# Optimization experiments

Measured on AMD Instinct MI355X. Metric: run time of the kernel, lower is better.

The kernel has to match this reference:

```python
import jax, jax.numpy as jnp
import numpy as np

EMBED_DIM = 1024
NUM_HEADS = 16
HEAD_DIM = EMBED_DIM // NUM_HEADS
SCALING = HEAD_DIM ** -0.5


def setup_inputs() -> dict:
    key = jax.random.key(0)
    ks = jax.random.split(key, 9)
    T, B, E = 2048, 4, EMBED_DIM
    s = 0.02
    return {
        "query": jax.random.normal(ks[0], (T, B, E), dtype=jnp.float32),
        "Wq": jax.random.normal(ks[1], (E, E), dtype=jnp.float32) * s,
        "bq": jnp.zeros((E,), dtype=jnp.float32),
        "Wk": jax.random.normal(ks[2], (E, E), dtype=jnp.float32) * s,
        "bk": jnp.zeros((E,), dtype=jnp.float32),
        "Wv": jax.random.normal(ks[3], (E, E), dtype=jnp.float32) * s,
        "bv": jnp.zeros((E,), dtype=jnp.float32),
        "Wo": jax.random.normal(ks[4], (E, E), dtype=jnp.float32) * s,
        "bo": jnp.zeros((E,), dtype=jnp.float32),
    }


def reference(query, Wq, bq, Wk, bk, Wv, bv, Wo, bo):
    # query: [T, B, E]; torch Linear: x @ W.T + b
    T, B, E = query.shape
    H, D = NUM_HEADS, HEAD_DIM
    q = (query @ Wq.T + bq) * SCALING
    k = query @ Wk.T + bk
    v = query @ Wv.T + bv
    # [T, B, E] -> [B*H, T, D]
    def split_heads(x):
        return x.reshape(T, B * H, D).transpose(1, 0, 2)
    q, k, v = split_heads(q), split_heads(k), split_heads(v)
    attn_weights = jnp.einsum("btd,bsd->bts", q, k)  # [B*H, T, T]
    attn_probs = jax.nn.softmax(attn_weights, axis=-1)
    attn = jnp.einsum("bts,bsd->btd", attn_probs, v)  # [B*H, T, D]
    attn = attn.transpose(1, 0, 2).reshape(T, B, E)
    return attn @ Wo.T + bo
```

## Files before the change

kernel.cpp:

```cpp
#include <hip/hip_runtime.h>
#include <stdint.h>

#define TSEQ   2048
#define BATCH  4
#define NHEAD  16
#define HDIM   64
#define EMB    1024
#define MROWS  (TSEQ * BATCH)
#define QKV_N  (3 * EMB)
#define SCALE_Q 0.125f
#define LOG2E  1.4426950408889634f

typedef __bf16  bf16x8  __attribute__((ext_vector_type(8)));
typedef __bf16  bf16x2  __attribute__((ext_vector_type(2)));
typedef short   s16x8   __attribute__((ext_vector_type(8)));
typedef float   f32x4   __attribute__((ext_vector_type(4)));
typedef float   f32x16  __attribute__((ext_vector_type(16)));

__device__ __forceinline__ uint16_t b16c(float f) {
    __bf16 h = (__bf16)f;
    return __builtin_bit_cast(uint16_t, h);
}
__device__ __forceinline__ uint32_t pk2(float a, float b) {
    bf16x2 h; h[0] = (__bf16)a; h[1] = (__bf16)b;
    return __builtin_bit_cast(uint32_t, h);
}
__device__ __forceinline__ float exp2hw(float x) {
    float r; asm("v_exp_f32 %0, %1" : "=v"(r) : "v"(x)); return r;
}
__device__ __forceinline__ bf16x8 ldfrag(const uint16_t* p) {
    return __builtin_bit_cast(bf16x8, *(const s16x8*)p);
}
__device__ __forceinline__ f32x4 MFMA(bf16x8 a, bf16x8 b, f32x4 c) {
    return __builtin_amdgcn_mfma_f32_16x16x32_bf16(a, b, c, 0, 0, 0);
}
__device__ __forceinline__ f32x16 MFMA32(bf16x8 a, bf16x8 b, f32x16 c) {
    return __builtin_amdgcn_mfma_f32_32x32x16_bf16(a, b, c, 0, 0, 0);
}

#define GLOAD_LDS16(g, l) \
    __builtin_amdgcn_global_load_lds((const __attribute__((address_space(1))) void*)(g), \
                                     (__attribute__((address_space(3))) void*)(l), 16, 0, 0)

__global__ void cvt_f2b4(const float* __restrict__ src, uint16_t* __restrict__ dst, int n4) {
    int i = blockIdx.x * blockDim.x + threadIdx.x;
    if (i >= n4) return;
    float4 v = ((const float4*)src)[i];
    ushort4 o;
    o.x = b16c(v.x); o.y = b16c(v.y); o.z = b16c(v.z); o.w = b16c(v.w);
    ((ushort4*)dst)[i] = o;
}

__global__ void cvt_wqkv(const float* __restrict__ Wq, const float* __restrict__ Wk,
                         const float* __restrict__ Wv, const float* __restrict__ bq,
                         const float* __restrict__ bk, const float* __restrict__ bv,
                         uint16_t* __restrict__ Wqkv, float* __restrict__ bqkv, int n4) {
    int i = blockIdx.x * blockDim.x + threadIdx.x;
    if (i < QKV_N) {
        float bval;
        if (i < EMB)            bval = bq[i] * SCALE_Q;
        else if (i < 2 * EMB)   bval = bk[i - EMB];
        else                    bval = bv[i - 2 * EMB];
        bqkv[i] = bval;
    }
    if (i >= n4) return;
    int e = i * 4;
    int n = e >> 10;
    int k = e & 1023;
    const float* src; float sc;
    if (n < EMB)            { src = Wq + ((size_t)n << 10) + k;             sc = SCALE_Q; }
    else if (n < 2 * EMB)   { src = Wk + ((size_t)(n - EMB) << 10) + k;     sc = 1.f; }
    else                    { src = Wv + ((size_t)(n - 2 * EMB) << 10) + k; sc = 1.f; }
    float4 v = *(const float4*)src;
    ushort4 o;
    o.x = b16c(v.x * sc); o.y = b16c(v.y * sc); o.z = b16c(v.z * sc); o.w = b16c(v.w * sc);
    ((ushort4*)Wqkv)[i] = o;
}

template <typename CT>
__global__ __launch_bounds__(256) void gemm_bt(
        const uint16_t* __restrict__ A, const uint16_t* __restrict__ Bt,
        const float* __restrict__ bias, CT* __restrict__ C,
        int M, int N, int K, int tiles_n) {
    __shared__ uint16_t As[128 * 32];
    __shared__ uint16_t Bs[128 * 32];

    const int nwg = gridDim.x;
    const int bid0 = blockIdx.x;
    const int bid = (bid0 & 7) * (nwg >> 3) + (bid0 >> 3);
    const int tm = bid / tiles_n, tn = bid % tiles_n;
    const int tid = threadIdx.x;
    const int l = tid & 63, w = tid >> 6;
    const int wm = w >> 1, wn = w & 1;
    const int fr = l & 15, fq = l >> 4;

    f32x4 acc[4][4] = {};

    const int row_a = tid >> 2;
    const int kblk  = (tid & 3) << 3;
    const uint16_t* gA0 = A  + (size_t)(tm * 128 + row_a) * K + kblk;
    const uint16_t* gB0 = Bt + (size_t)(tn * 128 + row_a) * K + kblk;
    const uint16_t* gA1 = gA0 + (size_t)64 * K;
    const uint16_t* gB1 = gB0 + (size_t)64 * K;
    uint16_t* lA0 = As + w * 512;
    uint16_t* lA1 = As + 2048 + w * 512;
    uint16_t* lB0 = Bs + w * 512;
    uint16_t* lB1 = Bs + 2048 + w * 512;

    for (int k0 = 0; k0 < K; k0 += 32) {
        GLOAD_LDS16(gA0 + k0, lA0);
        GLOAD_LDS16(gA1 + k0, lA1);
        GLOAD_LDS16(gB0 + k0, lB0);
        GLOAD_LDS16(gB1 + k0, lB1);
        __syncthreads();

        bf16x8 a[4], b[4];
#pragma unroll
        for (int i = 0; i < 4; i++)
            a[i] = ldfrag(&As[(wm * 64 + i * 16 + fr) * 32 + fq * 8]);
#pragma unroll
        for (int i = 0; i < 4; i++)
            b[i] = ldfrag(&Bs[(wn * 64 + i * 16 + fr) * 32 + fq * 8]);
#pragma unroll
        for (int i = 0; i < 4; i++)
#pragma unroll
            for (int j = 0; j < 4; j++)
                acc[i][j] = MFMA(a[i], b[j], acc[i][j]);
        __syncthreads();
    }

#pragma unroll
    for (int j = 0; j < 4; j++) {
        const int col = tn * 128 + wn * 64 + j * 16 + fr;
        const float bv = bias[col];
#pragma unroll
        for (int i = 0; i < 4; i++) {
#pragma unroll
            for (int r = 0; r < 4; r++) {
                const int row = tm * 128 + wm * 64 + i * 16 + fq * 4 + r;
                const float v = acc[i][j][r] + bv;
                if constexpr (sizeof(CT) == 2) C[(size_t)row * N + col] = (CT)b16c(v);
                else                           C[(size_t)row * N + col] = (CT)v;
            }
        }
    }
}

__device__ __forceinline__ int swze(int row, int colE) {
    return (row << 6) + (colE ^ ((((row & 7) ^ ((row >> 3) & 7)) & 7) << 3));
}

__device__ __forceinline__ void softmax_half(
        f32x16& s0, f32x16& s1, float& mrun, float& lrun,
        f32x16& oa, f32x16& ob, bf16x8* pf) {
    float t0 = s0[0], t1 = s0[1], t2 = s0[2], t3 = s0[3];
#pragma unroll
    for (int i = 4; i < 16; i += 4) {
        t0 = fmaxf(t0, s0[i]);     t1 = fmaxf(t1, s0[i + 1]);
        t2 = fmaxf(t2, s0[i + 2]); t3 = fmaxf(t3, s0[i + 3]);
    }
#pragma unroll
    for (int i = 0; i < 16; i += 4) {
        t0 = fmaxf(t0, s1[i]);     t1 = fmaxf(t1, s1[i + 1]);
        t2 = fmaxf(t2, s1[i + 2]); t3 = fmaxf(t3, s1[i + 3]);
    }
    float mx = fmaxf(fmaxf(t0, t1), fmaxf(t2, t3));
    {
        auto rm = __builtin_amdgcn_permlane32_swap(__float_as_int(mx), __float_as_int(mx), false, false);
        mx = fmaxf(__int_as_float(rm[0]), __int_as_float(rm[1]));
    }
    if (!__all(mx <= mrun + 8.f)) {
        float mnew = fmaxf(mrun, mx);
        float scl = exp2hw((mrun - mnew) * LOG2E);
        mrun = mnew;
        lrun *= scl;
#pragma unroll
        for (int i = 0; i < 16; i++) { oa[i] *= scl; ob[i] *= scl; }
    }
    const float mm = mrun * LOG2E;
#pragma unroll
    for (int i = 0; i < 16; i++) s0[i] = exp2hw(__builtin_fmaf(s0[i], LOG2E, -mm));
#pragma unroll
    for (int i = 0; i < 16; i++) s1[i] = exp2hw(__builtin_fmaf(s1[i], LOG2E, -mm));
    float p0 = 0.f, p1 = 0.f, p2 = 0.f, p3 = 0.f;
#pragma unroll
    for (int i = 0; i < 16; i += 4) {
        p0 += s0[i]; p1 += s0[i + 1]; p2 += s0[i + 2]; p3 += s0[i + 3];
        p0 += s1[i]; p1 += s1[i + 1]; p2 += s1[i + 2]; p3 += s1[i + 3];
    }
    float rs = (p0 + p1) + (p2 + p3);
    {
        auto rr2 = __builtin_amdgcn_permlane32_swap(__float_as_int(rs), __float_as_int(rs), false, false);
        rs = __int_as_float(rr2[0]) + __int_as_float(rr2[1]);
    }
    lrun += rs;

    uint32_t pk[16];
#pragma unroll
    for (int rr = 0; rr < 8; rr++) {
        pk[rr]     = pk2(s0[2 * rr], s0[2 * rr + 1]);
        pk[8 + rr] = pk2(s1[2 * rr], s1[2 * rr + 1]);
    }
#pragma unroll
    for (int kt = 0; kt < 4; kt++) {
        const int b0 = (kt >> 1) * 8 + (kt & 1) * 4;
        auto r02 = __builtin_amdgcn_permlane32_swap((int)pk[b0 + 0], (int)pk[b0 + 2], false, false);
        auto r13 = __builtin_amdgcn_permlane32_swap((int)pk[b0 + 1], (int)pk[b0 + 3], false, false);
        union { uint32_t u[4]; bf16x8 v; } cv;
        cv.u[0] = (uint32_t)r02[0]; cv.u[1] = (uint32_t)r13[0];
        cv.u[2] = (uint32_t)r02[1]; cv.u[3] = (uint32_t)r13[1];
        pf[kt] = cv.v;
    }
}

__global__ __launch_bounds__(256, 2) void flash_attn3(
        const uint16_t* __restrict__ qkv, uint16_t* __restrict__ attnb) {
    __shared__ __align__(16) uint16_t smem[16384];
    uint16_t* k0p = smem;
    uint16_t* k1p = smem + 4096;
    uint16_t* v0p = smem + 8192;
    uint16_t* v1p = smem + 12288;

    int bid = (int)blockIdx.x;
    bid = (bid & 7) * 64 + (bid >> 3);
    const int head = bid >> 3;
    const int qt   = bid & 7;
    const int b    = head >> 4, h = head & 15;
    const int tid  = threadIdx.x;
    const int l  = tid & 63, w = tid >> 6;
    const int q5 = l & 31;
    const int hi = l >> 5;
    const size_t tstep = (size_t)64 * 4 * 3072;

    const int qrowA = qt * 256 + w * 64 + q5;
    const uint16_t* qbA = qkv + ((size_t)(qrowA * 4 + b)) * 3072 + h * 64 + hi * 8;
    const uint16_t* qbB = qbA + (size_t)32 * 4 * 3072;
    bf16x8 qA[4], qB[4];
#pragma unroll
    for (int s = 0; s < 4; s++) { qA[s] = ldfrag(qbA + 16 * s); qB[s] = ldfrag(qbB + 16 * s); }

    const int r0 = w * 16 + (l >> 3);
    const int r1 = r0 + 8;
    const int cu0 = (((l & 7) ^ ((r0 & 7) ^ ((r0 >> 3) & 7))) & 7) << 3;
    const int cu1 = (((l & 7) ^ ((r1 & 7) ^ ((r1 >> 3) & 7))) & 7) << 3;
    const uint16_t* gk0 = qkv + ((size_t)(r0 * 4 + b)) * 3072 + 1024 + h * 64 + cu0;
    const uint16_t* gk1 = qkv + ((size_t)(r1 * 4 + b)) * 3072 + 1024 + h * 64 + cu1;
    const int kdst0 = w * 1024;
    const int kdst1 = w * 1024 + 512;

    const int skv  = (tid >> 3) * 2;
    const int scol = (tid & 7) * 8;
    const uint16_t* gv = qkv + ((size_t)(skv * 4 + b)) * 3072 + 2048 + h * 64 + scol;
    int voff[8];
#pragma unroll
    for (int j2 = 0; j2 < 8; j2++)
        voff[j2] = (scol + j2) * 64 + (skv ^ ((((j2 ^ (scol >> 3)) & 7)) << 3));

    GLOAD_LDS16(gk0, k0p + kdst0);
    GLOAD_LDS16(gk1, k0p + kdst1);
    {
        uint4 a0 = *(const uint4*)gv;
        uint4 a1 = *(const uint4*)(gv + 12288);
        const uint16_t* e0 = (const uint16_t*)&a0;
        const uint16_t* e1 = (const uint16_t*)&a1;
#pragma unroll
        for (int j2 = 0; j2 < 8; j2++)
            *(uint32_t*)&v0p[voff[j2]] = (uint32_t)e0[j2] | ((uint32_t)e1[j2] << 16);
    }
    gk0 += tstep; gk1 += tstep; gv += tstep;
    __syncthreads();

    f32x16 o0 = {}, o1 = {}, o2 = {}, o3 = {};
    float mrunA = -1e30f, lrunA = 0.f, mrunB = -1e30f, lrunB = 0.f;

    for (int t = 0; t < 32; t++) {
        const uint16_t* kb = (t & 1) ? k1p : k0p;
        const uint16_t* vb = (t & 1) ? v1p : v0p;
        uint16_t* kn = (t & 1) ? k0p : k1p;
        uint16_t* vn = (t & 1) ? v0p : v1p;

        uint4 a0, a1;
        if (t < 31) {
            GLOAD_LDS16(gk0, kn + kdst0);
            GLOAD_LDS16(gk1, kn + kdst1);
            a0 = *(const uint4*)gv;
            a1 = *(const uint4*)(gv + 12288);
            gk0 += tstep; gk1 += tstep; gv += tstep;
        }

        f32x16 sA0 = {}, sA1 = {}, sB0 = {}, sB1 = {};
#pragma unroll
        for (int s = 0; s < 4; s++) {
            bf16x8 kf0 = ldfrag(&kb[swze(q5,      16 * s + 8 * hi)]);
            bf16x8 kf1 = ldfrag(&kb[swze(32 + q5, 16 * s + 8 * hi)]);
            sA0 = MFMA32(kf0, qA[s], sA0);
            sA1 = MFMA32(kf1, qA[s], sA1);
            sB0 = MFMA32(kf0, qB[s], sB0);
            sB1 = MFMA32(kf1, qB[s], sB1);
        }

        bf16x8 pfA[4], pfB[4];
        softmax_half(sA0, sA1, mrunA, lrunA, o0, o1, pfA);
        softmax_half(sB0, sB1, mrunB, lrunB, o2, o3, pfB);

#pragma unroll
        for (int kt = 0; kt < 4; kt++) {
            bf16x8 vf0 = ldfrag(&vb[swze(q5,      16 * kt + 8 * hi)]);
            bf16x8 vf1 = ldfrag(&vb[swze(32 + q5, 16 * kt + 8 * hi)]);
            o0 = MFMA32(vf0, pfA[kt], o0);
            o1 = MFMA32(vf1, pfA[kt], o1);
            o2 = MFMA32(vf0, pfB[kt], o2);
            o3 = MFMA32(vf1, pfB[kt], o3);
        }

        if (t < 31) {
            const uint16_t* e0 = (const uint16_t*)&a0;
            const uint16_t* e1 = (const uint16_t*)&a1;
#pragma unroll
            for (int j2 = 0; j2 < 8; j2++)
                *(uint32_t*)&vn[voff[j2]] = (uint32_t)e0[j2] | ((uint32_t)e1[j2] << 16);
        }
        __syncthreads();
    }

    uint16_t* OstA = smem + w * 4096;
    uint16_t* OstB = OstA + 2048;
#pragma unroll
    for (int half = 0; half < 2; half++) {
        uint16_t* Ost = half ? OstB : OstA;
        const float inv = 1.f / (half ? lrunB : lrunA);
#pragma unroll
        for (int dt = 0; dt < 2; dt++) {
            const f32x16& ov = half ? (dt ? o3 : o2) : (dt ? o1 : o0);
#pragma unroll
            for (int a = 0; a < 4; a++) {
#pragma unroll
                for (int cp = 0; cp < 2; cp++) {
                    const int r = a * 4 + cp * 2;
                    uint32_t dw = pk2(ov[r] * inv, ov[r + 1] * inv);
                    const int d0 = dt * 32 + a * 8 + hi * 4 + cp * 2;
                    *(uint32_t*)&Ost[swze(q5, d0)] = dw;
                }
            }
        }
    }
    const int rq = l >> 1;
#pragma unroll
    for (int half = 0; half < 2; half++) {
        uint16_t* Ost = half ? OstB : OstA;
        const int qrow2 = qt * 256 + w * 64 + half * 32 + rq;
        uint16_t* ob = attnb + ((size_t)(qrow2 * 4 + b)) * 1024 + h * 64;
#pragma unroll
        for (int i = 0; i < 4; i++) {
            const int c4 = (l & 1) * 4 + i;
            uint4 vv = *(const uint4*)&Ost[swze(rq, c4 * 8)];
            *(uint4*)(ob + c4 * 8) = vv;
        }
    }
}

extern "C" void kernel_launch(void* const* d_in, const int* in_sizes, int n_in,
                              void* d_out, int out_size, void* d_ws, size_t ws_size,
                              hipStream_t stream) {
    const float* X  = (const float*)d_in[0];
    const float* Wq = (const float*)d_in[1];
    const float* bq = (const float*)d_in[2];
    const float* Wk = (const float*)d_in[3];
    const float* bk = (const float*)d_in[4];
    const float* Wv = (const float*)d_in[5];
    const float* bv = (const float*)d_in[6];
    const float* Wo = (const float*)d_in[7];
    const float* bo = (const float*)d_in[8];
    float* out = (float*)d_out;

    uint8_t* ws = (uint8_t*)d_ws;
    uint16_t* Xbf   = (uint16_t*)(ws);
    uint16_t* Wqkv  = (uint16_t*)(ws + 16777216);
    uint16_t* Wobf  = (uint16_t*)(ws + 23068672);
    float*    bqkv  = (float*)   (ws + 25165824);
    uint16_t* qkv   = (uint16_t*)(ws + 25178112);
    uint16_t* attnb = (uint16_t*)(ws + 75509760);

    cvt_f2b4<<<(MROWS * EMB / 4 + 255) / 256, 256, 0, stream>>>(X, Xbf, MROWS * EMB / 4);
    cvt_f2b4<<<(EMB * EMB / 4 + 255) / 256, 256, 0, stream>>>(Wo, Wobf, EMB * EMB / 4);
    cvt_wqkv<<<(QKV_N * EMB / 4 + 255) / 256, 256, 0, stream>>>(
        Wq, Wk, Wv, bq, bk, bv, Wqkv, bqkv, QKV_N * EMB / 4);

    gemm_bt<uint16_t><<<(MROWS / 128) * (QKV_N / 128), 256, 0, stream>>>(
        Xbf, Wqkv, bqkv, qkv, MROWS, QKV_N, EMB, QKV_N / 128);

    flash_attn3<<<512, 256, 0, stream>>>(qkv, attnb);

    gemm_bt<float><<<(MROWS / 128) * (EMB / 128), 256, 0, stream>>>(
        attnb, Wobf, bo, out, MROWS, EMB, EMB, EMB / 128);
}
```

Baseline: 218.6 us.

## Add 256x256 four-stage pipelined QKV GEMM and interleave softmax with PV MFMAs

Replaces the generic 128x128 GEMM for the QKV projection with a dedicated 512-thread kernel using 256x256 tiles, 32x32x16 MFMAs, a four-deep global_load_lds ring buffer with explicit vmcnt waits, and priority boosts around the MFMA blocks. In the attention kernel, the PV MFMAs for the first query half are issued between the two softmax passes so matrix work overlaps the exp and max work, and the QK loop gets setprio. The softmax row max is rewritten as a chain of three-input maxes so it can map to v_max3. The larger tile raises LDS use (128KB) and register pressure, which may limit occupancy.

Result: no change. 219.2 us (+0.3%).

```diff
diff --git a/kernel.cpp b/kernel.cpp
--- a/kernel.cpp
+++ b/kernel.cpp
@@ -27,6 +27,9 @@
 }
 __device__ __forceinline__ float exp2hw(float x) {
     float r; asm("v_exp_f32 %0, %1" : "=v"(r) : "v"(x)); return r;
+}
+__device__ __forceinline__ float max3f(float a, float b, float c) {
+    return fmaxf(fmaxf(a, b), c);
 }
 __device__ __forceinline__ bf16x8 ldfrag(const uint16_t* p) {
     return __builtin_bit_cast(bf16x8, *(const s16x8*)p);
@@ -146,6 +149,110 @@
     }
 }
 
+#define SWZK(r) ((((r) & 3) ^ (((r) >> 2) & 3)))
+
+__global__ __launch_bounds__(512, 2) void gemm_qkv(
+        const uint16_t* __restrict__ A, const uint16_t* __restrict__ Bt,
+        const float* __restrict__ bias, uint16_t* __restrict__ C) {
+    __shared__ __align__(16) uint16_t lds[4 * 16384];
+
+    const int bid0 = blockIdx.x;
+    const int bid = (bid0 & 7) * 48 + (bid0 >> 3);
+    const int tm = bid / 12, tn = bid % 12;
+    const int tid = threadIdx.x;
+    const int w = tid >> 6, l = tid & 63;
+    const int wm = w >> 2, wn = w & 3;
+    const int l5 = l & 31, hi = l >> 5;
+
+    const uint16_t* gA[2]; const uint16_t* gB[2];
+    int ldsA[2], ldsB[2];
+#pragma unroll
+    for (int i = 0; i < 2; i++) {
+        int c = i * 512 + tid;
+        int row = c >> 2, fqp = c & 3;
+        gA[i] = A  + (size_t)(tm * 256 + row) * 1024 + ((fqp ^ SWZK(row)) * 8);
+        gB[i] = Bt + (size_t)(tn * 256 + row) * 1024 + ((fqp ^ SWZK(row)) * 8);
+        ldsA[i] = (i * 512 + w * 64) * 8;
+        ldsB[i] = 8192 + (i * 512 + w * 64) * 8;
+    }
+
+    int aoff[4][2], boff[2][2];
+#pragma unroll
+    for (int mf = 0; mf < 4; mf++) {
+        int row = wm * 128 + mf * 32 + l5;
+#pragma unroll
+        for (int ks = 0; ks < 2; ks++)
+            aoff[mf][ks] = row * 32 + (((ks * 2 + hi) ^ SWZK(row)) * 8);
+    }
+#pragma unroll
+    for (int nf = 0; nf < 2; nf++) {
+        int row = wn * 64 + nf * 32 + l5;
+#pragma unroll
+        for (int ks = 0; ks < 2; ks++)
+            boff[nf][ks] = 8192 + row * 32 + (((ks * 2 + hi) ^ SWZK(row)) * 8);
+    }
+
+    f32x16 acc[4][2] = {};
+
+#define STAGE_T(t, s)                                            \
+    {                                                            \
+        uint16_t* base_ = lds + (s) * 16384;                     \
+        GLOAD_LDS16(gA[0] + (t) * 32, base_ + ldsA[0]);          \
+        GLOAD_LDS16(gB[0] + (t) * 32, base_ + ldsB[0]);          \
+        GLOAD_LDS16(gA[1] + (t) * 32, base_ + ldsA[1]);          \
+        GLOAD_LDS16(gB[1] + (t) * 32, base_ + ldsB[1]);          \
+    }
+
+    STAGE_T(0, 0); STAGE_T(1, 1); STAGE_T(2, 2);
+    asm volatile("s_waitcnt vmcnt(8)" ::: "memory");
+    __builtin_amdgcn_s_barrier();
+    __builtin_amdgcn_sched_barrier(0);
+
+    for (int j = 0; j < 32; j++) {
+        const int s = j & 3;
+        if (j + 3 < 32) STAGE_T(j + 3, (j + 3) & 3);
+        const uint16_t* sl = lds + s * 16384;
+
+#pragma unroll
+        for (int ks = 0; ks < 2; ks++) {
+            bf16x8 af[4], bfg[2];
+#pragma unroll
+            for (int mf = 0; mf < 4; mf++) af[mf] = ldfrag(sl + aoff[mf][ks]);
+#pragma unroll
+            for (int nf = 0; nf < 2; nf++) bfg[nf] = ldfrag(sl + boff[nf][ks]);
+            __builtin_amdgcn_s_setprio(1);
+#pragma unroll
+            for (int mf = 0; mf < 4; mf++)
+#pragma unroll
+                for (int nf = 0; nf < 2; nf++)
+                    acc[mf][nf] = MFMA32(af[mf], bfg[nf], acc[mf][nf]);
+            __builtin_amdgcn_s_setprio(0);
+        }
+
+        __builtin_amdgcn_sched_barrier(0);
+        if (j < 29)       asm volatile("s_waitcnt vmcnt(8)" ::: "memory");
+        else if (j == 29) asm volatile("s_waitcnt vmcnt(4)" ::: "memory");
+        else              asm volatile("s_waitcnt vmcnt(0)" ::: "memory");
+        __builtin_amdgcn_s_barrier();
+        __builtin_amdgcn_sched_barrier(0);
+    }
+
+#pragma unroll
+    for (int nf = 0; nf < 2; nf++) {
+        const int col = tn * 256 + wn * 64 + nf * 32 + l5;
+        const float bv = bias[col];
+#pragma unroll
+        for (int mf = 0; mf < 4; mf++) {
+#pragma unroll
+            for (int r = 0; r < 16; r++) {
+                const int row = tm * 256 + wm * 128 + mf * 32 + (r & 3) + 8 * (r >> 2) + 4 * hi;
+                C[(size_t)row * 3072 + col] = b16c(acc[mf][nf][r] + bv);
+            }
+        }
+    }
+#undef STAGE_T
+}
+
 __device__ __forceinline__ int swze(int row, int colE) {
     return (row << 6) + (colE ^ ((((row & 7) ^ ((row >> 3) & 7)) & 7) << 3));
 }
@@ -153,18 +260,16 @@
 __device__ __forceinline__ void softmax_half(
         f32x16& s0, f32x16& s1, float& mrun, float& lrun,
         f32x16& oa, f32x16& ob, bf16x8* pf) {
-    float t0 = s0[0], t1 = s0[1], t2 = s0[2], t3 = s0[3];
-#pragma unroll
-    for (int i = 4; i < 16; i += 4) {
-        t0 = fmaxf(t0, s0[i]);     t1 = fmaxf(t1, s0[i + 1]);
-        t2 = fmaxf(t2, s0[i + 2]); t3 = fmaxf(t3, s0[i + 3]);
-    }
-#pragma unroll
-    for (int i = 0; i < 16; i += 4) {
-        t0 = fmaxf(t0, s1[i]);     t1 = fmaxf(t1, s1[i + 1]);
-        t2 = fmaxf(t2, s1[i + 2]); t3 = fmaxf(t3, s1[i + 3]);
-    }
-    float mx = fmaxf(fmaxf(t0, t1), fmaxf(t2, t3));
+    float t0 = max3f(s0[0], s0[4], s0[8]);
+    float t1 = max3f(s0[1], s0[5], s0[9]);
+    float t2 = max3f(s0[2], s0[6], s0[10]);
+    float t3 = max3f(s0[3], s0[7], s0[11]);
+    t0 = max3f(t0, s0[12], s1[0]);  t1 = max3f(t1, s0[13], s1[1]);
+    t2 = max3f(t2, s0[14], s1[2]);  t3 = max3f(t3, s0[15], s1[3]);
+    t0 = max3f(t0, s1[4], s1[8]);   t1 = max3f(t1, s1[5], s1[9]);
+    t2 = max3f(t2, s1[6], s1[10]);  t3 = max3f(t3, s1[7], s1[11]);
+    t0 = max3f(t0, s1[12], t1);     t2 = max3f(t2, s1[13], t3);
+    float mx = max3f(t0, s1[14], max3f(t2, s1[15], t0));
     {
         auto rm = __builtin_amdgcn_permlane32_swap(__float_as_int(mx), __float_as_int(mx), false, false);
         mx = fmaxf(__int_as_float(rm[0]), __int_as_float(rm[1]));
@@ -213,7 +318,7 @@
     }
 }
 
-__global__ __launch_bounds__(256, 2) void flash_attn3(
+__global__ __launch_bounds__(256, 2) void flash_attn4(
         const uint16_t* __restrict__ qkv, uint16_t* __restrict__ attnb) {
     __shared__ __align__(16) uint16_t smem[16384];
     uint16_t* k0p = smem;
@@ -289,6 +394,7 @@
         }
 
         f32x16 sA0 = {}, sA1 = {}, sB0 = {}, sB1 = {};
+        __builtin_amdgcn_s_setprio(1);
 #pragma unroll
         for (int s = 0; s < 4; s++) {
             bf16x8 kf0 = ldfrag(&kb[swze(q5,      16 * s + 8 * hi)]);
@@ -298,20 +404,33 @@
             sB0 = MFMA32(kf0, qB[s], sB0);
             sB1 = MFMA32(kf1, qB[s], sB1);
         }
+        __builtin_amdgcn_s_setprio(0);
 
         bf16x8 pfA[4], pfB[4];
         softmax_half(sA0, sA1, mrunA, lrunA, o0, o1, pfA);
+
+        bf16x8 vfr0[4], vfr1[4];
+#pragma unroll
+        for (int kt = 0; kt < 4; kt++) {
+            vfr0[kt] = ldfrag(&vb[swze(q5,      16 * kt + 8 * hi)]);
+            vfr1[kt] = ldfrag(&vb[swze(32 + q5, 16 * kt + 8 * hi)]);
+        }
+        __builtin_amdgcn_s_setprio(1);
+#pragma unroll
+        for (int kt = 0; kt < 4; kt++) {
+            o0 = MFMA32(vfr0[kt], pfA[kt], o0);
+            o1 = MFMA32(vfr1[kt], pfA[kt], o1);
+        }
+        __builtin_amdgcn_s_setprio(0);
+
         softmax_half(sB0, sB1, mrunB, lrunB, o2, o3, pfB);
-
+        __builtin_amdgcn_s_setprio(1);
 #pragma unroll
         for (int kt = 0; kt < 4; kt++) {
-            bf16x8 vf0 = ldfrag(&vb[swze(q5,      16 * kt + 8 * hi)]);
-            bf16x8 vf1 = ldfrag(&vb[swze(32 + q5, 16 * kt + 8 * hi)]);
-            o0 = MFMA32(vf0, pfA[kt], o0);
-            o1 = MFMA32(vf1, pfA[kt], o1);
-            o2 = MFMA32(vf0, pfB[kt], o2);
-            o3 = MFMA32(vf1, pfB[kt], o3);
-        }
+            o2 = MFMA32(vfr0[kt], pfB[kt], o2);
+            o3 = MFMA32(vfr1[kt], pfB[kt], o3);
+        }
+        __builtin_amdgcn_s_setprio(0);
 
         if (t < 31) {
             const uint16_t* e0 = (const uint16_t*)&a0;
@@ -386,10 +505,9 @@
     cvt_wqkv<<<(QKV_N * EMB / 4 + 255) / 256, 256, 0, stream>>>(
         Wq, Wk, Wv, bq, bk, bv, Wqkv, bqkv, QKV_N * EMB / 4);
 
-    gemm_bt<uint16_t><<<(MROWS / 128) * (QKV_N / 128), 256, 0, stream>>>(
-        Xbf, Wqkv, bqkv, qkv, MROWS, QKV_N, EMB, QKV_N / 128);
-
-    flash_attn3<<<512, 256, 0, stream>>>(qkv, attnb);
+    gemm_qkv<<<384, 512, 0, stream>>>(Xbf, Wqkv, bqkv, qkv);
+
+    flash_attn4<<<512, 256, 0, stream>>>(qkv, attnb);
 
     gemm_bt<float><<<(MROWS / 128) * (EMB / 128), 256, 0, stream>>>(
         attnb, Wobf, bo, out, MROWS, EMB, EMB, EMB / 128);
```
